# Optimization experiments

Measured on AMD Instinct MI355X. Metric: run time of the kernel, lower is better.

Reference implementation:

```python
import jax, jax.numpy as jnp
import numpy as np

N, K, W = 500000, 512, 64


def setup_inputs() -> dict:
    key = jax.random.key(0)
    kx, kc = jax.random.split(key)
    X = jax.random.normal(kx, (N, W), dtype=jnp.float32)
    # nn.init.uniform_(codebook.weight, a=-1.0, b=1.0)
    codebook = jax.random.uniform(kc, (K, W), dtype=jnp.float32, minval=-1.0, maxval=1.0)
    return {"X": X, "codebook": codebook}


def reference(X, codebook):
    # torch.cdist (p=2): pairwise Euclidean distances [N, K]
    x2 = jnp.sum(X * X, axis=-1, keepdims=True)          # [N, 1]
    c2 = jnp.sum(codebook * codebook, axis=-1)           # [K]
    d2 = x2 - 2.0 * (X @ codebook.T) + c2[None, :]        # [N, K]
    dist = jnp.sqrt(jnp.maximum(d2, 0.0))
    idx = jnp.argmin(dist, axis=-1)                       # [N] int
    min_dists = jnp.min(dist, axis=-1)                    # [N] == gather(dist, idx)
    return idx, min_dists
```

## Files before the change

### kernel.cpp

```cpp
#include <hip/hip_runtime.h>

#define N_POINTS 500000
#define K_CENT   512
#define W_DIM    64
#define N_JOBS   ((N_POINTS + 63) / 64)

typedef _Float16 half8 __attribute__((ext_vector_type(8)));
typedef float    f32x16 __attribute__((ext_vector_type(16)));

__global__ void cvt_kernel(const float* __restrict__ cb,
                           _Float16* __restrict__ cbf) {
    int id = blockIdx.x * 256 + threadIdx.x;
    if (id >= K_CENT * 8) return;
    int c = id >> 3, o = (id & 7) * 8;
    int t = c >> 5, r = c & 31;
    int s = o >> 4, half = (o >> 3) & 1;
    int lane = half * 32 + r;
    const float* src = cb + (size_t)c * W_DIM + o;
    half8 h, l;
#pragma unroll
    for (int j = 0; j < 8; ++j) {
        float w = -2.0f * src[j];
        _Float16 hh = (_Float16)w;
        h[j] = hh;
        l[j] = (_Float16)(w - (float)hh);
    }
    size_t base_h = ((size_t)(t * 2 + 0) * 4 + s) * 512 + (size_t)lane * 8;
    size_t base_l = ((size_t)(t * 2 + 1) * 4 + s) * 512 + (size_t)lane * 8;
    *(half8*)(cbf + base_h) = h;
    *(half8*)(cbf + base_l) = l;
}

__global__ void c2_kernel(const float* __restrict__ cb, float* __restrict__ c2) {
    int c = blockIdx.x * 256 + threadIdx.x;
    if (c >= K_CENT) return;
    const float4* row = (const float4*)(cb + (size_t)c * W_DIM);
    double s = 0.0;
#pragma unroll
    for (int j = 0; j < W_DIM / 4; ++j) {
        float4 v = row[j];
        s += (double)v.x * v.x + (double)v.y * v.y + (double)v.z * v.z + (double)v.w * v.w;
    }
    c2[c] = (float)s;
}

#define MFMA_CHUNK(T, CURH, CURL, NXTH, NXTL, QC, QN, A0, A1)                      \
    {                                                                              \
        int t_ = (T);                                                              \
        if (t_ < 15) {                                                             \
            const _Float16* nb = cbf + (size_t)(t_ + 1) * 4096 + (size_t)lane * 8; \
            NXTH[0] = *(const half8*)(nb + 0 * 512);                               \
            NXTH[1] = *(const half8*)(nb + 1 * 512);                               \
            NXTH[2] = *(const half8*)(nb + 2 * 512);                               \
            NXTH[3] = *(const half8*)(nb + 3 * 512);                               \
            NXTL[0] = *(const half8*)(nb + 2048 + 0 * 512);                        \
            NXTL[1] = *(const half8*)(nb + 2048 + 1 * 512);                        \
            NXTL[2] = *(const half8*)(nb + 2048 + 2 * 512);                        \
            NXTL[3] = *(const half8*)(nb + 2048 + 3 * 512);                        \
            QN = *(const f32x16*)&c2s[(t_ + 1) * 32 + half16];                     \
        }                                                                          \
        A0 = __builtin_amdgcn_mfma_f32_32x32x16_f16(CURH[0], b0h[0], QC, 0, 0, 0); \
        A1 = __builtin_amdgcn_mfma_f32_32x32x16_f16(CURH[0], b1h[0], QC, 0, 0, 0); \
        A0 = __builtin_amdgcn_mfma_f32_32x32x16_f16(CURL[0], b0h[0], A0, 0, 0, 0); \
        A1 = __builtin_amdgcn_mfma_f32_32x32x16_f16(CURL[0], b1h[0], A1, 0, 0, 0); \
        A0 = __builtin_amdgcn_mfma_f32_32x32x16_f16(CURH[0], b0l[0], A0, 0, 0, 0); \
        A1 = __builtin_amdgcn_mfma_f32_32x32x16_f16(CURH[0], b1l[0], A1, 0, 0, 0); \
        _Pragma("unroll")                                                          \
        for (int s = 1; s < 4; ++s) {                                              \
            A0 = __builtin_amdgcn_mfma_f32_32x32x16_f16(CURH[s], b0h[s], A0, 0, 0, 0); \
            A1 = __builtin_amdgcn_mfma_f32_32x32x16_f16(CURH[s], b1h[s], A1, 0, 0, 0); \
            A0 = __builtin_amdgcn_mfma_f32_32x32x16_f16(CURL[s], b0h[s], A0, 0, 0, 0); \
            A1 = __builtin_amdgcn_mfma_f32_32x32x16_f16(CURL[s], b1h[s], A1, 0, 0, 0); \
            A0 = __builtin_amdgcn_mfma_f32_32x32x16_f16(CURH[s], b0l[s], A0, 0, 0, 0); \
            A1 = __builtin_amdgcn_mfma_f32_32x32x16_f16(CURH[s], b1l[s], A1, 0, 0, 0); \
        }                                                                          \
    }

#define ARGMIN_TILE(AM, BD, BI, T_)                                            \
    {                                                                          \
        float m01 = fminf(AM[0], AM[1]),   m23 = fminf(AM[2], AM[3]);          \
        float m45 = fminf(AM[4], AM[5]),   m67 = fminf(AM[6], AM[7]);          \
        float m89 = fminf(AM[8], AM[9]),   mab = fminf(AM[10], AM[11]);        \
        float mcd = fminf(AM[12], AM[13]), mef = fminf(AM[14], AM[15]);        \
        float n0 = fminf(m01, m23),  n1 = fminf(m45, m67);                     \
        float n2 = fminf(m89, mab),  n3 = fminf(mcd, mef);                     \
        float m  = fminf(fminf(n0, n1), fminf(n2, n3));                        \
        int ji = 15;                                                           \
        ji = (AM[14] == m) ? 14 : ji; ji = (AM[13] == m) ? 13 : ji;            \
        ji = (AM[12] == m) ? 12 : ji; ji = (AM[11] == m) ? 11 : ji;            \
        ji = (AM[10] == m) ? 10 : ji; ji = (AM[9]  == m) ?  9 : ji;            \
        ji = (AM[8]  == m) ?  8 : ji; ji = (AM[7]  == m) ?  7 : ji;            \
        ji = (AM[6]  == m) ?  6 : ji; ji = (AM[5]  == m) ?  5 : ji;            \
        ji = (AM[4]  == m) ?  4 : ji; ji = (AM[3]  == m) ?  3 : ji;            \
        ji = (AM[2]  == m) ?  2 : ji; ji = (AM[1]  == m) ?  1 : ji;            \
        ji = (AM[0]  == m) ?  0 : ji;                                          \
        int ci = (T_) * 32 + half4 + ((ji >> 2) << 3) + (ji & 3);              \
        bool imp = m < BD;                                                     \
        BD = imp ? m : BD;                                                     \
        BI = imp ? ci : BI;                                                    \
    }

#define ARGMIN_CHUNK(T, A0, A1)                                                \
    {                                                                          \
        ARGMIN_TILE(A0, bd0, bi0, T)                                           \
        ARGMIN_TILE(A1, bd1, bi1, T)                                           \
    }

__global__ __launch_bounds__(256, 2)
void kmeans_mfma(const float* __restrict__ X,
                 const _Float16* __restrict__ cbf,
                 const float* __restrict__ c2,
                 float* __restrict__ out_idx,
                 float* __restrict__ out_dist) {
    __shared__ float c2s[K_CENT];
    int tid = threadIdx.x;
    {
        int i = tid;
        int t = i >> 5, h = (i >> 4) & 1, j = i & 15;
        c2s[i] = c2[t * 32 + h * 4 + ((j >> 2) << 3) + (j & 3)];
        i = tid + 256;
        t = i >> 5; h = (i >> 4) & 1; j = i & 15;
        c2s[i] = c2[t * 32 + h * 4 + ((j >> 2) << 3) + (j & 3)];
    }
    __syncthreads();

    int wave = tid >> 6;
    int lane = tid & 63;
    int half = lane >> 5;
    int l31  = lane & 31;
    int kb   = half * 8;
    int half4  = half * 4;
    int half16 = half * 16;

    int job = blockIdx.x * 4 + wave;
    if (job >= N_JOBS) return;

    int  p0 = job * 64 + l31;
    bool v1ok = (job * 64 + 32) < N_POINTS;
    int  p1 = v1ok ? (p0 + 32) : p0;

    half8 b0h[4], b0l[4], b1h[4], b1l[4];
    float x20 = 0.f, x21 = 0.f;
#pragma unroll
    for (int s = 0; s < 4; ++s) {
        const float4* xa = (const float4*)(X + (size_t)p0 * W_DIM + s * 16 + kb);
        float4 f0 = xa[0], f1 = xa[1];
        float fa[8] = {f0.x, f0.y, f0.z, f0.w, f1.x, f1.y, f1.z, f1.w};
        const float4* xb = (const float4*)(X + (size_t)p1 * W_DIM + s * 16 + kb);
        float4 g0 = xb[0], g1 = xb[1];
        float fb[8] = {g0.x, g0.y, g0.z, g0.w, g1.x, g1.y, g1.z, g1.w};
#pragma unroll
        for (int j = 0; j < 8; ++j) {
            _Float16 h0 = (_Float16)fa[j];
            b0h[s][j] = h0;
            b0l[s][j] = (_Float16)(fa[j] - (float)h0);
            x20 = fmaf(fa[j], fa[j], x20);
            _Float16 h1 = (_Float16)fb[j];
            b1h[s][j] = h1;
            b1l[s][j] = (_Float16)(fb[j] - (float)h1);
            x21 = fmaf(fb[j], fb[j], x21);
        }
    }
    x20 += __shfl_xor(x20, 32);
    x21 += __shfl_xor(x21, 32);

    float bd0 = 3.4e38f, bd1 = 3.4e38f;
    int   bi0 = 0,       bi1 = 0;

    half8 ahA[4], alA[4], ahB[4], alB[4];
    f32x16 qP, qQ, accP0, accP1, accQ0, accQ1;
    {
        const _Float16* ab = cbf + (size_t)lane * 8;
        ahA[0] = *(const half8*)(ab + 0 * 512);
        ahA[1] = *(const half8*)(ab + 1 * 512);
        ahA[2] = *(const half8*)(ab + 2 * 512);
        ahA[3] = *(const half8*)(ab + 3 * 512);
        alA[0] = *(const half8*)(ab + 2048 + 0 * 512);
        alA[1] = *(const half8*)(ab + 2048 + 1 * 512);
        alA[2] = *(const half8*)(ab + 2048 + 2 * 512);
        alA[3] = *(const half8*)(ab + 2048 + 3 * 512);
    }
    qP = *(const f32x16*)&c2s[0 * 32 + half16];

    MFMA_CHUNK(0, ahA, alA, ahB, alB, qP, qQ, accP0, accP1)

#pragma unroll 1
    for (int tt = 0; tt < 7; ++tt) {
        MFMA_CHUNK(2 * tt + 1, ahB, alB, ahA, alA, qQ, qP, accQ0, accQ1)
        ARGMIN_CHUNK(2 * tt, accP0, accP1)
        MFMA_CHUNK(2 * tt + 2, ahA, alA, ahB, alB, qP, qQ, accP0, accP1)
        ARGMIN_CHUNK(2 * tt + 1, accQ0, accQ1)
    }
    MFMA_CHUNK(15, ahB, alB, ahA, alA, qQ, qP, accQ0, accQ1)
    ARGMIN_CHUNK(14, accP0, accP1)
    ARGMIN_CHUNK(15, accQ0, accQ1)

    {
        float od = __shfl_xor(bd0, 32); int oi = __shfl_xor(bi0, 32);
        if (od < bd0 || (od == bd0 && oi < bi0)) { bd0 = od; bi0 = oi; }
        od = __shfl_xor(bd1, 32); oi = __shfl_xor(bi1, 32);
        if (od < bd1 || (od == bd1 && oi < bi1)) { bd1 = od; bi1 = oi; }
    }

    if (half == 0) {
        out_idx[p0]  = (float)bi0;
        out_dist[p0] = sqrtf(fmaxf(bd0 + x20, 0.f));
        if (v1ok) {
            out_idx[p1]  = (float)bi1;
            out_dist[p1] = sqrtf(fmaxf(bd1 + x21, 0.f));
        }
    }
}

extern "C" void kernel_launch(void* const* d_in, const int* in_sizes, int n_in,
                              void* d_out, int out_size, void* d_ws, size_t ws_size,
                              hipStream_t stream) {
    const float* X  = (const float*)d_in[0];
    const float* cb = (const float*)d_in[1];
    float* out      = (float*)d_out;

    _Float16* cbf = (_Float16*)d_ws;
    float*    c2  = (float*)(cbf + (size_t)K_CENT * W_DIM * 2);

    hipLaunchKernelGGL(cvt_kernel, dim3((K_CENT * 8 + 255) / 256), dim3(256), 0, stream, cb, cbf);
    hipLaunchKernelGGL(c2_kernel, dim3((K_CENT + 255) / 256), dim3(256), 0, stream, cb, c2);

    hipLaunchKernelGGL(kmeans_mfma, dim3((N_JOBS + 3) / 4), dim3(256), 0, stream,
                       X, cbf, c2, out, out + N_POINTS);
}
```

Baseline: 105.2 us.

## Process three point tiles per wave and use tree-based argmin index recovery

Each wave now handles three 32-point tiles instead of two, so every codebook fragment loaded into registers feeds three MFMA chains rather than two. The codebook double buffer is replaced by a single buffer that is reloaded after each chunk's MFMAs are issued. The per-tile argmin index search changes from a 15-step linear select chain to a 4-level walk back down the min tree. More accumulators and X registers raise register pressure, and reloading into one buffer may expose load latency.

After: 114.7 us. 9.0% more time.

```diff
diff --git a/kernel.cpp b/kernel.cpp
--- a/kernel.cpp
+++ b/kernel.cpp
@@ -3,7 +3,8 @@
 #define N_POINTS 500000
 #define K_CENT   512
 #define W_DIM    64
-#define N_JOBS   ((N_POINTS + 63) / 64)
+#define N_TILES  (N_POINTS / 32)
+#define N_JOBS3  ((N_TILES + 2) / 3)
 
 typedef _Float16 half8 __attribute__((ext_vector_type(8)));
 typedef float    f32x16 __attribute__((ext_vector_type(16)));
@@ -44,66 +45,95 @@
     c2[c] = (float)s;
 }
 
-#define MFMA_CHUNK(T, CURH, CURL, NXTH, NXTL, QC, QN, A0, A1)                      \
+#define MFMA3_CHUNK(QC, A0, A1, A2)                                                \
+    {                                                                              \
+        A0 = __builtin_amdgcn_mfma_f32_32x32x16_f16(ah[0], b0h[0], QC, 0, 0, 0);   \
+        A1 = __builtin_amdgcn_mfma_f32_32x32x16_f16(ah[0], b1h[0], QC, 0, 0, 0);   \
+        A2 = __builtin_amdgcn_mfma_f32_32x32x16_f16(ah[0], b2h[0], QC, 0, 0, 0);   \
+        A0 = __builtin_amdgcn_mfma_f32_32x32x16_f16(al[0], b0h[0], A0, 0, 0, 0);   \
+        A1 = __builtin_amdgcn_mfma_f32_32x32x16_f16(al[0], b1h[0], A1, 0, 0, 0);   \
+        A2 = __builtin_amdgcn_mfma_f32_32x32x16_f16(al[0], b2h[0], A2, 0, 0, 0);   \
+        A0 = __builtin_amdgcn_mfma_f32_32x32x16_f16(ah[0], b0l[0], A0, 0, 0, 0);   \
+        A1 = __builtin_amdgcn_mfma_f32_32x32x16_f16(ah[0], b1l[0], A1, 0, 0, 0);   \
+        A2 = __builtin_amdgcn_mfma_f32_32x32x16_f16(ah[0], b2l[0], A2, 0, 0, 0);   \
+        _Pragma("unroll")                                                          \
+        for (int s = 1; s < 4; ++s) {                                              \
+            A0 = __builtin_amdgcn_mfma_f32_32x32x16_f16(ah[s], b0h[s], A0, 0, 0, 0); \
+            A1 = __builtin_amdgcn_mfma_f32_32x32x16_f16(ah[s], b1h[s], A1, 0, 0, 0); \
+            A2 = __builtin_amdgcn_mfma_f32_32x32x16_f16(ah[s], b2h[s], A2, 0, 0, 0); \
+            A0 = __builtin_amdgcn_mfma_f32_32x32x16_f16(al[s], b0h[s], A0, 0, 0, 0); \
+            A1 = __builtin_amdgcn_mfma_f32_32x32x16_f16(al[s], b1h[s], A1, 0, 0, 0); \
+            A2 = __builtin_amdgcn_mfma_f32_32x32x16_f16(al[s], b2h[s], A2, 0, 0, 0); \
+            A0 = __builtin_amdgcn_mfma_f32_32x32x16_f16(ah[s], b0l[s], A0, 0, 0, 0); \
+            A1 = __builtin_amdgcn_mfma_f32_32x32x16_f16(ah[s], b1l[s], A1, 0, 0, 0); \
+            A2 = __builtin_amdgcn_mfma_f32_32x32x16_f16(ah[s], b2l[s], A2, 0, 0, 0); \
+        }                                                                          \
+    }
+
+#define PREFETCH(T, QN)                                                            \
     {                                                                              \
         int t_ = (T);                                                              \
-        if (t_ < 15) {                                                             \
-            const _Float16* nb = cbf + (size_t)(t_ + 1) * 4096 + (size_t)lane * 8; \
-            NXTH[0] = *(const half8*)(nb + 0 * 512);                               \
-            NXTH[1] = *(const half8*)(nb + 1 * 512);                               \
-            NXTH[2] = *(const half8*)(nb + 2 * 512);                               \
-            NXTH[3] = *(const half8*)(nb + 3 * 512);                               \
-            NXTL[0] = *(const half8*)(nb + 2048 + 0 * 512);                        \
-            NXTL[1] = *(const half8*)(nb + 2048 + 1 * 512);                        \
-            NXTL[2] = *(const half8*)(nb + 2048 + 2 * 512);                        \
-            NXTL[3] = *(const half8*)(nb + 2048 + 3 * 512);                        \
-            QN = *(const f32x16*)&c2s[(t_ + 1) * 32 + half16];                     \
-        }                                                                          \
-        A0 = __builtin_amdgcn_mfma_f32_32x32x16_f16(CURH[0], b0h[0], QC, 0, 0, 0); \
-        A1 = __builtin_amdgcn_mfma_f32_32x32x16_f16(CURH[0], b1h[0], QC, 0, 0, 0); \
-        A0 = __builtin_amdgcn_mfma_f32_32x32x16_f16(CURL[0], b0h[0], A0, 0, 0, 0); \
-        A1 = __builtin_amdgcn_mfma_f32_32x32x16_f16(CURL[0], b1h[0], A1, 0, 0, 0); \
-        A0 = __builtin_amdgcn_mfma_f32_32x32x16_f16(CURH[0], b0l[0], A0, 0, 0, 0); \
-        A1 = __builtin_amdgcn_mfma_f32_32x32x16_f16(CURH[0], b1l[0], A1, 0, 0, 0); \
-        _Pragma("unroll")                                                          \
-        for (int s = 1; s < 4; ++s) {                                              \
-            A0 = __builtin_amdgcn_mfma_f32_32x32x16_f16(CURH[s], b0h[s], A0, 0, 0, 0); \
-            A1 = __builtin_amdgcn_mfma_f32_32x32x16_f16(CURH[s], b1h[s], A1, 0, 0, 0); \
-            A0 = __builtin_amdgcn_mfma_f32_32x32x16_f16(CURL[s], b0h[s], A0, 0, 0, 0); \
-            A1 = __builtin_amdgcn_mfma_f32_32x32x16_f16(CURL[s], b1h[s], A1, 0, 0, 0); \
-            A0 = __builtin_amdgcn_mfma_f32_32x32x16_f16(CURH[s], b0l[s], A0, 0, 0, 0); \
-            A1 = __builtin_amdgcn_mfma_f32_32x32x16_f16(CURH[s], b1l[s], A1, 0, 0, 0); \
+        if (t_ < 16) {                                                             \
+            const _Float16* nb = cbf + (size_t)t_ * 4096 + (size_t)lane * 8;       \
+            ah[0] = *(const half8*)(nb + 0 * 512);                                 \
+            ah[1] = *(const half8*)(nb + 1 * 512);                                 \
+            ah[2] = *(const half8*)(nb + 2 * 512);                                 \
+            ah[3] = *(const half8*)(nb + 3 * 512);                                 \
+            al[0] = *(const half8*)(nb + 2048 + 0 * 512);                          \
+            al[1] = *(const half8*)(nb + 2048 + 1 * 512);                          \
+            al[2] = *(const half8*)(nb + 2048 + 2 * 512);                          \
+            al[3] = *(const half8*)(nb + 2048 + 3 * 512);                          \
+            QN = *(const f32x16*)&c2s[t_ * 32 + half16];                           \
         }                                                                          \
     }
 
 #define ARGMIN_TILE(AM, BD, BI, T_)                                            \
     {                                                                          \
-        float m01 = fminf(AM[0], AM[1]),   m23 = fminf(AM[2], AM[3]);          \
-        float m45 = fminf(AM[4], AM[5]),   m67 = fminf(AM[6], AM[7]);          \
-        float m89 = fminf(AM[8], AM[9]),   mab = fminf(AM[10], AM[11]);        \
-        float mcd = fminf(AM[12], AM[13]), mef = fminf(AM[14], AM[15]);        \
-        float n0 = fminf(m01, m23),  n1 = fminf(m45, m67);                     \
-        float n2 = fminf(m89, mab),  n3 = fminf(mcd, mef);                     \
-        float m  = fminf(fminf(n0, n1), fminf(n2, n3));                        \
-        int ji = 15;                                                           \
-        ji = (AM[14] == m) ? 14 : ji; ji = (AM[13] == m) ? 13 : ji;            \
-        ji = (AM[12] == m) ? 12 : ji; ji = (AM[11] == m) ? 11 : ji;            \
-        ji = (AM[10] == m) ? 10 : ji; ji = (AM[9]  == m) ?  9 : ji;            \
-        ji = (AM[8]  == m) ?  8 : ji; ji = (AM[7]  == m) ?  7 : ji;            \
-        ji = (AM[6]  == m) ?  6 : ji; ji = (AM[5]  == m) ?  5 : ji;            \
-        ji = (AM[4]  == m) ?  4 : ji; ji = (AM[3]  == m) ?  3 : ji;            \
-        ji = (AM[2]  == m) ?  2 : ji; ji = (AM[1]  == m) ?  1 : ji;            \
-        ji = (AM[0]  == m) ?  0 : ji;                                          \
+        float a0 = fminf(AM[0], AM[1]),   a1 = fminf(AM[2], AM[3]);            \
+        float a2 = fminf(AM[4], AM[5]),   a3 = fminf(AM[6], AM[7]);            \
+        float a4 = fminf(AM[8], AM[9]),   a5 = fminf(AM[10], AM[11]);          \
+        float a6 = fminf(AM[12], AM[13]), a7 = fminf(AM[14], AM[15]);          \
+        float b0 = fminf(a0, a1), b1 = fminf(a2, a3);                          \
+        float b2 = fminf(a4, a5), b3 = fminf(a6, a7);                          \
+        float c0 = fminf(b0, b1), c1 = fminf(b2, b3);                          \
+        float m  = fminf(c0, c1);                                              \
+        bool  L3 = (m == c0);                                                  \
+        float bL = L3 ? b0 : b2;                                               \
+        bool  L2 = (m == bL);                                                  \
+        float aL = L3 ? (L2 ? a0 : a2) : (L2 ? a4 : a6);                       \
+        bool  L1 = (m == aL);                                                  \
+        float vE = L3 ? (L2 ? (L1 ? AM[0] : AM[2]) : (L1 ? AM[4] : AM[6]))     \
+                      : (L2 ? (L1 ? AM[8] : AM[10]) : (L1 ? AM[12] : AM[14])); \
+        bool  L0 = (m == vE);                                                  \
+        int ji = (L3 ? 0 : 8) | (L2 ? 0 : 4) | (L1 ? 0 : 2) | (L0 ? 0 : 1);    \
         int ci = (T_) * 32 + half4 + ((ji >> 2) << 3) + (ji & 3);              \
         bool imp = m < BD;                                                     \
         BD = imp ? m : BD;                                                     \
         BI = imp ? ci : BI;                                                    \
     }
 
-#define ARGMIN_CHUNK(T, A0, A1)                                                \
+#define ARGMIN3(T, A0, A1, A2)                                                 \
     {                                                                          \
         ARGMIN_TILE(A0, bd0, bi0, T)                                           \
         ARGMIN_TILE(A1, bd1, bi1, T)                                           \
+        ARGMIN_TILE(A2, bd2, bi2, T)                                           \
+    }
+
+#define LOADB(BH, BL, P, X2)                                                   \
+    {                                                                          \
+        _Pragma("unroll")                                                      \
+        for (int s = 0; s < 4; ++s) {                                          \
+            const float4* xp = (const float4*)(X + (size_t)(P) * W_DIM + s * 16 + kb); \
+            float4 f0 = xp[0], f1 = xp[1];                                     \
+            float fa[8] = {f0.x, f0.y, f0.z, f0.w, f1.x, f1.y, f1.z, f1.w};    \
+            _Pragma("unroll")                                                  \
+            for (int j = 0; j < 8; ++j) {                                      \
+                _Float16 hh = (_Float16)fa[j];                                 \
+                BH[s][j] = hh;                                                 \
+                BL[s][j] = (_Float16)(fa[j] - (float)hh);                      \
+                X2 = fmaf(fa[j], fa[j], X2);                                   \
+            }                                                                  \
+        }                                                                      \
     }
 
 __global__ __launch_bounds__(256, 2)
@@ -112,7 +142,7 @@
                  const float* __restrict__ c2,
                  float* __restrict__ out_idx,
                  float* __restrict__ out_dist) {
-    __shared__ float c2s[K_CENT];
+    __shared__ __align__(64) float c2s[K_CENT];
     int tid = threadIdx.x;
     {
         int i = tid;
@@ -133,81 +163,60 @@
     int half16 = half * 16;
 
     int job = blockIdx.x * 4 + wave;
-    if (job >= N_JOBS) return;
-
-    int  p0 = job * 64 + l31;
-    bool v1ok = (job * 64 + 32) < N_POINTS;
-    int  p1 = v1ok ? (p0 + 32) : p0;
-
-    half8 b0h[4], b0l[4], b1h[4], b1l[4];
-    float x20 = 0.f, x21 = 0.f;
-#pragma unroll
-    for (int s = 0; s < 4; ++s) {
-        const float4* xa = (const float4*)(X + (size_t)p0 * W_DIM + s * 16 + kb);
-        float4 f0 = xa[0], f1 = xa[1];
-        float fa[8] = {f0.x, f0.y, f0.z, f0.w, f1.x, f1.y, f1.z, f1.w};
-        const float4* xb = (const float4*)(X + (size_t)p1 * W_DIM + s * 16 + kb);
-        float4 g0 = xb[0], g1 = xb[1];
-        float fb[8] = {g0.x, g0.y, g0.z, g0.w, g1.x, g1.y, g1.z, g1.w};
-#pragma unroll
-        for (int j = 0; j < 8; ++j) {
-            _Float16 h0 = (_Float16)fa[j];
-            b0h[s][j] = h0;
-            b0l[s][j] = (_Float16)(fa[j] - (float)h0);
-            x20 = fmaf(fa[j], fa[j], x20);
-            _Float16 h1 = (_Float16)fb[j];
-            b1h[s][j] = h1;
-            b1l[s][j] = (_Float16)(fb[j] - (float)h1);
-            x21 = fmaf(fb[j], fb[j], x21);
-        }
-    }
+    if (job >= N_JOBS3) return;
+
+    int t0 = job * 3;
+    int  p0 = t0 * 32 + l31;
+    bool ok1 = (t0 + 1) < N_TILES;
+    bool ok2 = (t0 + 2) < N_TILES;
+    int  p1 = ok1 ? (p0 + 32) : p0;
+    int  p2 = ok2 ? (p0 + 64) : p0;
+
+    half8 b0h[4], b0l[4], b1h[4], b1l[4], b2h[4], b2l[4];
+    float x20 = 0.f, x21 = 0.f, x22 = 0.f;
+    LOADB(b0h, b0l, p0, x20)
+    LOADB(b1h, b1l, p1, x21)
+    LOADB(b2h, b2l, p2, x22)
     x20 += __shfl_xor(x20, 32);
     x21 += __shfl_xor(x21, 32);
-
-    float bd0 = 3.4e38f, bd1 = 3.4e38f;
-    int   bi0 = 0,       bi1 = 0;
-
-    half8 ahA[4], alA[4], ahB[4], alB[4];
-    f32x16 qP, qQ, accP0, accP1, accQ0, accQ1;
-    {
-        const _Float16* ab = cbf + (size_t)lane * 8;
-        ahA[0] = *(const half8*)(ab + 0 * 512);
-        ahA[1] = *(const half8*)(ab + 1 * 512);
-        ahA[2] = *(const half8*)(ab + 2 * 512);
-        ahA[3] = *(const half8*)(ab + 3 * 512);
-        alA[0] = *(const half8*)(ab + 2048 + 0 * 512);
-        alA[1] = *(const half8*)(ab + 2048 + 1 * 512);
-        alA[2] = *(const half8*)(ab + 2048 + 2 * 512);
-        alA[3] = *(const half8*)(ab + 2048 + 3 * 512);
-    }
-    qP = *(const f32x16*)&c2s[0 * 32 + half16];
-
-    MFMA_CHUNK(0, ahA, alA, ahB, alB, qP, qQ, accP0, accP1)
+    x22 += __shfl_xor(x22, 32);
+
+    float bd0 = 3.4e38f, bd1 = 3.4e38f, bd2 = 3.4e38f;
+    int   bi0 = 0,       bi1 = 0,       bi2 = 0;
+
+    half8 ah[4], al[4];
+    f32x16 qP, qQ, accP0, accP1, accP2, accQ0, accQ1, accQ2;
+    PREFETCH(0, qP)
 
 #pragma unroll 1
-    for (int tt = 0; tt < 7; ++tt) {
-        MFMA_CHUNK(2 * tt + 1, ahB, alB, ahA, alA, qQ, qP, accQ0, accQ1)
-        ARGMIN_CHUNK(2 * tt, accP0, accP1)
-        MFMA_CHUNK(2 * tt + 2, ahA, alA, ahB, alB, qP, qQ, accP0, accP1)
-        ARGMIN_CHUNK(2 * tt + 1, accQ0, accQ1)
-    }
-    MFMA_CHUNK(15, ahB, alB, ahA, alA, qQ, qP, accQ0, accQ1)
-    ARGMIN_CHUNK(14, accP0, accP1)
-    ARGMIN_CHUNK(15, accQ0, accQ1)
+    for (int tt = 0; tt < 8; ++tt) {
+        MFMA3_CHUNK(qP, accP0, accP1, accP2)
+        PREFETCH(2 * tt + 1, qQ)
+        ARGMIN3(2 * tt, accP0, accP1, accP2)
+        MFMA3_CHUNK(qQ, accQ0, accQ1, accQ2)
+        PREFETCH(2 * tt + 2, qP)
+        ARGMIN3(2 * tt + 1, accQ0, accQ1, accQ2)
+    }
 
     {
         float od = __shfl_xor(bd0, 32); int oi = __shfl_xor(bi0, 32);
         if (od < bd0 || (od == bd0 && oi < bi0)) { bd0 = od; bi0 = oi; }
         od = __shfl_xor(bd1, 32); oi = __shfl_xor(bi1, 32);
         if (od < bd1 || (od == bd1 && oi < bi1)) { bd1 = od; bi1 = oi; }
+        od = __shfl_xor(bd2, 32); oi = __shfl_xor(bi2, 32);
+        if (od < bd2 || (od == bd2 && oi < bi2)) { bd2 = od; bi2 = oi; }
     }
 
     if (half == 0) {
         out_idx[p0]  = (float)bi0;
         out_dist[p0] = sqrtf(fmaxf(bd0 + x20, 0.f));
-        if (v1ok) {
+        if (ok1) {
             out_idx[p1]  = (float)bi1;
             out_dist[p1] = sqrtf(fmaxf(bd1 + x21, 0.f));
+        }
+        if (ok2) {
+            out_idx[p2]  = (float)bi2;
+            out_dist[p2] = sqrtf(fmaxf(bd2 + x22, 0.f));
         }
     }
 }
@@ -225,6 +234,6 @@
     hipLaunchKernelGGL(cvt_kernel, dim3((K_CENT * 8 + 255) / 256), dim3(256), 0, stream, cb, cbf);
     hipLaunchKernelGGL(c2_kernel, dim3((K_CENT + 255) / 256), dim3(256), 0, stream, cb, c2);
 
-    hipLaunchKernelGGL(kmeans_mfma, dim3((N_JOBS + 3) / 4), dim3(256), 0, stream,
+    hipLaunchKernelGGL(kmeans_mfma, dim3((N_JOBS3 + 3) / 4), dim3(256), 0, stream,
                        X, cbf, c2, out, out + N_POINTS);
 }
```

## Split MFMA accumulation into main and correction chains, drop software pipelining, tree argmin

Applied to the files above, without the earlier changes.

Each tile's dot products now go into two independent accumulator chains: the hi*hi terms plus c2, and the split-precision correction terms starting from zero. The two are summed before the argmin. This halves the dependent MFMA chain length per accumulator. The argmin index search now walks back down the min tree instead of doing 15 compares. The double-buffered accumulator scheme that overlapped argmin of one tile with MFMAs of the next is removed, which lowers register pressure but serialises compute and argmin within a wave.

New measurement: 112.5 us. +7.0%, slower.

```diff
diff --git a/kernel.cpp b/kernel.cpp
--- a/kernel.cpp
+++ b/kernel.cpp
@@ -44,7 +44,7 @@
     c2[c] = (float)s;
 }
 
-#define MFMA_CHUNK(T, CURH, CURL, NXTH, NXTL, QC, QN, A0, A1)                      \
+#define MFMA_CHUNK(T, CURH, CURL, NXTH, NXTL, QC, QN)                              \
     {                                                                              \
         int t_ = (T);                                                              \
         if (t_ < 15) {                                                             \
@@ -59,51 +59,60 @@
             NXTL[3] = *(const half8*)(nb + 2048 + 3 * 512);                        \
             QN = *(const f32x16*)&c2s[(t_ + 1) * 32 + half16];                     \
         }                                                                          \
-        A0 = __builtin_amdgcn_mfma_f32_32x32x16_f16(CURH[0], b0h[0], QC, 0, 0, 0); \
-        A1 = __builtin_amdgcn_mfma_f32_32x32x16_f16(CURH[0], b1h[0], QC, 0, 0, 0); \
-        A0 = __builtin_amdgcn_mfma_f32_32x32x16_f16(CURL[0], b0h[0], A0, 0, 0, 0); \
-        A1 = __builtin_amdgcn_mfma_f32_32x32x16_f16(CURL[0], b1h[0], A1, 0, 0, 0); \
-        A0 = __builtin_amdgcn_mfma_f32_32x32x16_f16(CURH[0], b0l[0], A0, 0, 0, 0); \
-        A1 = __builtin_amdgcn_mfma_f32_32x32x16_f16(CURH[0], b1l[0], A1, 0, 0, 0); \
+        am0 = __builtin_amdgcn_mfma_f32_32x32x16_f16(CURH[0], b0h[0], QC, 0, 0, 0);  \
+        am1 = __builtin_amdgcn_mfma_f32_32x32x16_f16(CURH[0], b1h[0], QC, 0, 0, 0);  \
+        ac0 = __builtin_amdgcn_mfma_f32_32x32x16_f16(CURL[0], b0h[0], zro, 0, 0, 0); \
+        ac1 = __builtin_amdgcn_mfma_f32_32x32x16_f16(CURL[0], b1h[0], zro, 0, 0, 0); \
+        ac0 = __builtin_amdgcn_mfma_f32_32x32x16_f16(CURH[0], b0l[0], ac0, 0, 0, 0); \
+        ac1 = __builtin_amdgcn_mfma_f32_32x32x16_f16(CURH[0], b1l[0], ac1, 0, 0, 0); \
         _Pragma("unroll")                                                          \
         for (int s = 1; s < 4; ++s) {                                              \
-            A0 = __builtin_amdgcn_mfma_f32_32x32x16_f16(CURH[s], b0h[s], A0, 0, 0, 0); \
-            A1 = __builtin_amdgcn_mfma_f32_32x32x16_f16(CURH[s], b1h[s], A1, 0, 0, 0); \
-            A0 = __builtin_amdgcn_mfma_f32_32x32x16_f16(CURL[s], b0h[s], A0, 0, 0, 0); \
-            A1 = __builtin_amdgcn_mfma_f32_32x32x16_f16(CURL[s], b1h[s], A1, 0, 0, 0); \
-            A0 = __builtin_amdgcn_mfma_f32_32x32x16_f16(CURH[s], b0l[s], A0, 0, 0, 0); \
-            A1 = __builtin_amdgcn_mfma_f32_32x32x16_f16(CURH[s], b1l[s], A1, 0, 0, 0); \
+            am0 = __builtin_amdgcn_mfma_f32_32x32x16_f16(CURH[s], b0h[s], am0, 0, 0, 0); \
+            am1 = __builtin_amdgcn_mfma_f32_32x32x16_f16(CURH[s], b1h[s], am1, 0, 0, 0); \
+            ac0 = __builtin_amdgcn_mfma_f32_32x32x16_f16(CURL[s], b0h[s], ac0, 0, 0, 0); \
+            ac1 = __builtin_amdgcn_mfma_f32_32x32x16_f16(CURL[s], b1h[s], ac1, 0, 0, 0); \
+            ac0 = __builtin_amdgcn_mfma_f32_32x32x16_f16(CURH[s], b0l[s], ac0, 0, 0, 0); \
+            ac1 = __builtin_amdgcn_mfma_f32_32x32x16_f16(CURH[s], b1l[s], ac1, 0, 0, 0); \
         }                                                                          \
     }
 
-#define ARGMIN_TILE(AM, BD, BI, T_)                                            \
+#define ARGMIN_TILE(AM, AC, BD, BI, T_)                                        \
     {                                                                          \
-        float m01 = fminf(AM[0], AM[1]),   m23 = fminf(AM[2], AM[3]);          \
-        float m45 = fminf(AM[4], AM[5]),   m67 = fminf(AM[6], AM[7]);          \
-        float m89 = fminf(AM[8], AM[9]),   mab = fminf(AM[10], AM[11]);        \
-        float mcd = fminf(AM[12], AM[13]), mef = fminf(AM[14], AM[15]);        \
-        float n0 = fminf(m01, m23),  n1 = fminf(m45, m67);                     \
-        float n2 = fminf(m89, mab),  n3 = fminf(mcd, mef);                     \
-        float m  = fminf(fminf(n0, n1), fminf(n2, n3));                        \
-        int ji = 15;                                                           \
-        ji = (AM[14] == m) ? 14 : ji; ji = (AM[13] == m) ? 13 : ji;            \
-        ji = (AM[12] == m) ? 12 : ji; ji = (AM[11] == m) ? 11 : ji;            \
-        ji = (AM[10] == m) ? 10 : ji; ji = (AM[9]  == m) ?  9 : ji;            \
-        ji = (AM[8]  == m) ?  8 : ji; ji = (AM[7]  == m) ?  7 : ji;            \
-        ji = (AM[6]  == m) ?  6 : ji; ji = (AM[5]  == m) ?  5 : ji;            \
-        ji = (AM[4]  == m) ?  4 : ji; ji = (AM[3]  == m) ?  3 : ji;            \
-        ji = (AM[2]  == m) ?  2 : ji; ji = (AM[1]  == m) ?  1 : ji;            \
-        ji = (AM[0]  == m) ?  0 : ji;                                          \
+        float v0  = AM[0]  + AC[0],  v1  = AM[1]  + AC[1];                     \
+        float v2  = AM[2]  + AC[2],  v3  = AM[3]  + AC[3];                     \
+        float v4  = AM[4]  + AC[4],  v5  = AM[5]  + AC[5];                     \
+        float v6  = AM[6]  + AC[6],  v7  = AM[7]  + AC[7];                     \
+        float v8  = AM[8]  + AC[8],  v9  = AM[9]  + AC[9];                     \
+        float v10 = AM[10] + AC[10], v11 = AM[11] + AC[11];                    \
+        float v12 = AM[12] + AC[12], v13 = AM[13] + AC[13];                    \
+        float v14 = AM[14] + AC[14], v15 = AM[15] + AC[15];                    \
+        float a0 = fminf(v0, v1),   a1 = fminf(v2, v3);                        \
+        float a2 = fminf(v4, v5),   a3 = fminf(v6, v7);                        \
+        float a4 = fminf(v8, v9),   a5 = fminf(v10, v11);                      \
+        float a6 = fminf(v12, v13), a7 = fminf(v14, v15);                      \
+        float b0 = fminf(a0, a1), b1 = fminf(a2, a3);                          \
+        float b2 = fminf(a4, a5), b3 = fminf(a6, a7);                          \
+        float c0 = fminf(b0, b1), c1 = fminf(b2, b3);                          \
+        float m  = fminf(c0, c1);                                              \
+        bool  L3 = (m == c0);                                                  \
+        float bL = L3 ? b0 : b2;                                               \
+        bool  L2 = (m == bL);                                                  \
+        float aL = L3 ? (L2 ? a0 : a2) : (L2 ? a4 : a6);                       \
+        bool  L1 = (m == aL);                                                  \
+        float vE = L3 ? (L2 ? (L1 ? v0 : v2) : (L1 ? v4 : v6))                 \
+                      : (L2 ? (L1 ? v8 : v10) : (L1 ? v12 : v14));             \
+        bool  L0 = (m == vE);                                                  \
+        int ji = (L3 ? 0 : 8) | (L2 ? 0 : 4) | (L1 ? 0 : 2) | (L0 ? 0 : 1);    \
         int ci = (T_) * 32 + half4 + ((ji >> 2) << 3) + (ji & 3);              \
         bool imp = m < BD;                                                     \
         BD = imp ? m : BD;                                                     \
         BI = imp ? ci : BI;                                                    \
     }
 
-#define ARGMIN_CHUNK(T, A0, A1)                                                \
+#define ARGMIN_CHUNK(T)                                                        \
     {                                                                          \
-        ARGMIN_TILE(A0, bd0, bi0, T)                                           \
-        ARGMIN_TILE(A1, bd1, bi1, T)                                           \
+        ARGMIN_TILE(am0, ac0, bd0, bi0, T)                                     \
+        ARGMIN_TILE(am1, ac1, bd1, bi1, T)                                     \
     }
 
 __global__ __launch_bounds__(256, 2)
@@ -112,7 +121,7 @@
                  const float* __restrict__ c2,
                  float* __restrict__ out_idx,
                  float* __restrict__ out_dist) {
-    __shared__ float c2s[K_CENT];
+    __shared__ __align__(64) float c2s[K_CENT];
     int tid = threadIdx.x;
     {
         int i = tid;
@@ -167,8 +176,12 @@
     float bd0 = 3.4e38f, bd1 = 3.4e38f;
     int   bi0 = 0,       bi1 = 0;
 
+    f32x16 zro;
+#pragma unroll
+    for (int j = 0; j < 16; ++j) zro[j] = 0.f;
+
     half8 ahA[4], alA[4], ahB[4], alB[4];
-    f32x16 qP, qQ, accP0, accP1, accQ0, accQ1;
+    f32x16 qP, qQ, am0, am1, ac0, ac1;
     {
         const _Float16* ab = cbf + (size_t)lane * 8;
         ahA[0] = *(const half8*)(ab + 0 * 512);
@@ -182,18 +195,13 @@
     }
     qP = *(const f32x16*)&c2s[0 * 32 + half16];
 
-    MFMA_CHUNK(0, ahA, alA, ahB, alB, qP, qQ, accP0, accP1)
-
 #pragma unroll 1
-    for (int tt = 0; tt < 7; ++tt) {
-        MFMA_CHUNK(2 * tt + 1, ahB, alB, ahA, alA, qQ, qP, accQ0, accQ1)
-        ARGMIN_CHUNK(2 * tt, accP0, accP1)
-        MFMA_CHUNK(2 * tt + 2, ahA, alA, ahB, alB, qP, qQ, accP0, accP1)
-        ARGMIN_CHUNK(2 * tt + 1, accQ0, accQ1)
-    }
-    MFMA_CHUNK(15, ahB, alB, ahA, alA, qQ, qP, accQ0, accQ1)
-    ARGMIN_CHUNK(14, accP0, accP1)
-    ARGMIN_CHUNK(15, accQ0, accQ1)
+    for (int tt = 0; tt < 8; ++tt) {
+        MFMA_CHUNK(2 * tt,     ahA, alA, ahB, alB, qP, qQ)
+        ARGMIN_CHUNK(2 * tt)
+        MFMA_CHUNK(2 * tt + 1, ahB, alB, ahA, alA, qQ, qP)
+        ARGMIN_CHUNK(2 * tt + 1)
+    }
 
     {
         float od = __shfl_xor(bd0, 32); int oi = __shfl_xor(bi0, 32);
```
